# Performance work log

Measured on AMD Instinct MI355X. Metric: run time of the kernel, lower is better.

Reference implementation:

```python
import jax, jax.numpy as jnp
import numpy as np

B, CIN, HIN, WIN = 8192, 16, 6, 6
FM = 64                      # feature_maps
DK = FM // 2                 # 32
DV = FM // 2                 # 32
NH = FM // 2                 # 32 heads -> dkh = dvh = 1
OUT_CH = 5
HID = 128


def _conv2d(x, w, b, stride=1):
    # x: NCHW, w: OIHW, VALID padding (padding=(k-1)//2 = 0 for k=2)
    y = jax.lax.conv_general_dilated(
        x, w, window_strides=(stride, stride), padding='VALID',
        dimension_numbers=('NCHW', 'OIHW', 'NCHW'))
    return y + b[None, :, None, None]


def setup_inputs() -> dict:
    key = jax.random.key(0)
    ks = jax.random.split(key, 13)
    s = 0.1  # small init scale keeps softmax logits well-conditioned
    return {
        'x':      jax.random.normal(ks[0], (B, CIN, HIN, WIN), jnp.float32),
        # AugmentedConv: conv_out (out_channels - dv), qkv conv (2dk+dv), attn 1x1
        'conv_w': jax.random.normal(ks[1], (FM - DV, CIN, 2, 2), jnp.float32) * s,
        'conv_b': jax.random.normal(ks[2], (FM - DV,), jnp.float32) * s,
        'qkv_w':  jax.random.normal(ks[3], (2 * DK + DV, CIN, 2, 2), jnp.float32) * s,
        'qkv_b':  jax.random.normal(ks[4], (2 * DK + DV,), jnp.float32) * s,
        'attn_w': jax.random.normal(ks[5], (DV, DV, 1, 1), jnp.float32) * s,
        'attn_b': jax.random.normal(ks[6], (DV,), jnp.float32) * s,
        # DoubleDense: fm*5*5 -> hid -> hid//2 -> out
        'w1': jax.random.normal(ks[7], (HID, FM * 5 * 5), jnp.float32) * s,
        'b1': jax.random.normal(ks[8], (HID,), jnp.float32) * s,
        'w2': jax.random.normal(ks[9], (HID // 2, HID), jnp.float32) * s,
        'b2': jax.random.normal(ks[10], (HID // 2,), jnp.float32) * s,
        'w3': jax.random.normal(ks[11], (OUT_CH, HID // 2), jnp.float32) * s,
        'b3': jax.random.normal(ks[12], (OUT_CH,), jnp.float32) * s,
    }


def _forward(x, conv_w, conv_b, qkv_w, qkv_b, attn_w, attn_b, w1, b1, w2, b2, w3, b3):
    # ---- AugmentedConv ----
    conv_out = _conv2d(x, conv_w, conv_b)            # [B, FM-DV, 5, 5]
    qkv = _conv2d(x, qkv_w, qkv_b)                   # [B, 2DK+DV, 5, 5]
    b, _, h, w = qkv.shape
    q, k, v = jnp.split(qkv, [DK, 2 * DK], axis=1)
    dkh = DK // NH
    q = q * (dkh ** -0.5)
    flat_q = q.reshape(b, NH, dkh, h * w)            # [B, Nh, dkh, HW]
    flat_k = k.reshape(b, NH, dkh, h * w)
    flat_v = v.reshape(b, NH, DV // NH, h * w)
    # logits = q^T k over head-dim: [B, Nh, HW, HW]
    logits = jnp.einsum('bndi,bndj->bnij', flat_q, flat_k)
    weights = jax.nn.softmax(logits, axis=-1)
    # attn = weights @ v^T -> [B, Nh, HW, dvh]
    attn = jnp.einsum('bnij,bnjd->bnid', weights, flat_v.transpose(0, 1, 3, 2))
    # faithful to torch: raw reshape (B, Nh, dvh, H, W) then combine heads
    attn = attn.reshape(b, NH, DV // NH, h, w).reshape(b, DV, h, w)
    attn = _conv2d(attn, attn_w, attn_b)             # 1x1 conv
    y = jnp.concatenate([conv_out, attn], axis=1)    # [B, FM, 5, 5]
    # ---- ReLU + DoubleDense ----
    y = jax.nn.relu(y).reshape(b, -1)                # [B, FM*25]
    y = jax.nn.relu(y @ w1.T + b1)
    y = jax.nn.relu(y @ w2.T + b2)
    return y @ w3.T + b3                             # [B, OUT_CH]


def reference(x, conv_w, conv_b, qkv_w, qkv_b, attn_w, attn_b, w1, b1, w2, b2, w3, b3):
    return _forward(x, conv_w, conv_b, qkv_w, qkv_b, attn_w, attn_b,
                    w1, b1, w2, b2, w3, b3)
```

## Files before the change

kernel.cpp:

```cpp
#include <hip/hip_runtime.h>
#include <hip/hip_bf16.h>
#include <cstdint>
#include <cstddef>


typedef __attribute__((ext_vector_type(4))) float f32x4;
typedef __attribute__((ext_vector_type(2))) float f32x2;
typedef __attribute__((ext_vector_type(8))) __bf16 bf16x8;
typedef __attribute__((ext_vector_type(4))) __bf16 bf16x4;

#define LOG2E 1.4426950408889634f
#define ACT_STRIDE 1608
#define ACT_LDS_BYTES (32 * ACT_STRIDE * 2)
#define LDS_TOTAL (ACT_LDS_BYTES + 8 * 7168)

__device__ __forceinline__ float fast_exp2(float x) {
#if __has_builtin(__builtin_amdgcn_exp2f)
  return __builtin_amdgcn_exp2f(x);
#else
  return __expf(x * 0.6931471805599453f);
#endif
}

__device__ __forceinline__ f32x4 mfma16(bf16x8 a, bf16x8 b, f32x4 c) {
  return __builtin_amdgcn_mfma_f32_16x16x32_bf16(a, b, c, 0, 0, 0);
}

__global__ __launch_bounds__(64) void prep(
    const float* __restrict__ conv_w, const float* __restrict__ conv_b,
    const float* __restrict__ qkv_w,  const float* __restrict__ qkv_b,
    const float* __restrict__ attn_w,
    const float* __restrict__ w1, const float* __restrict__ w2,
    __hip_bfloat16* __restrict__ wqb, float* __restrict__ biasb,
    __hip_bfloat16* __restrict__ wab,
    __hip_bfloat16* __restrict__ w1bp, __hip_bfloat16* __restrict__ w2b) {
  const int t = threadIdx.x, tb = blockIdx.x;
  if (tb < 16) {
#pragma unroll
    for (int j = 0; j < 8; ++j) {
      int i = tb * 512 + j * 64 + t;
      float w = (i < 2048) ? conv_w[i] : qkv_w[i - 2048];
      if (i >= 4096 && i < 6144) w *= LOG2E;
      wqb[i] = __float2bfloat16(w);
    }
  } else if (tb == 16) {
#pragma unroll
    for (int j = 0; j < 16; ++j) wab[j * 64 + t] = __float2bfloat16(attn_w[j * 64 + t]);
    for (int i = t; i < 128; i += 64) {
      float b = (i < 32) ? conv_b[i] : qkv_b[i - 32];
      if (i >= 64 && i < 96) b *= LOG2E;
      biasb[i] = b;
    }
  } else if (tb < 145) {
    const int u = tb - 17;
    __shared__ float rowf[1600];
    const float* wr = w1 + u * 1600;
#pragma unroll
    for (int j = 0; j < 25; ++j) rowf[j * 64 + t] = wr[j * 64 + t];
    __hip_bfloat16* wo = w1bp + u * 1600;
#pragma unroll
    for (int j = 0; j < 25; ++j) {
      wo[j * 64 + t] = __float2bfloat16(rowf[t * 25 + j]);
    }
  } else {
#pragma unroll
    for (int j = 0; j < 64; ++j) {
      int i = (tb - 145) * 4096 + j * 64 + t;
      w2b[i] = __float2bfloat16(w2[i]);
    }
  }
}

__global__ __launch_bounds__(512) void kf(
    const float* __restrict__ x,
    const float* __restrict__ biasb,
    const __hip_bfloat16* __restrict__ wqb,
    const __hip_bfloat16* __restrict__ wab, const float* __restrict__ attn_b,
    const __hip_bfloat16* __restrict__ w1bp, const float* __restrict__ b1,
    const __hip_bfloat16* __restrict__ w2b, const float* __restrict__ b2,
    const float* __restrict__ w3, const float* __restrict__ b3,
    float* __restrict__ out) {
  extern __shared__ __align__(16) char lds_all[];
  const int t = threadIdx.x & 63;
  const int wv = threadIdx.x >> 6;
  const int l15 = t & 15, quad = t >> 4;

  __hip_bfloat16* act_lds = (__hip_bfloat16*)lds_all;
  char* my = lds_all + ACT_LDS_BYTES + wv * 7168;
  __bf16* xs  = (__bf16*)my;
  __bf16* as_ = (__bf16*)my;
  __bf16* qs  = (__bf16*)(my + 1600);

  bf16x8 bfr[8][2];
#pragma unroll
  for (int nt = 0; nt < 8; ++nt)
#pragma unroll
    for (int ks = 0; ks < 2; ++ks)
      bfr[nt][ks] = *(const bf16x8*)((const __bf16*)wqb + (nt * 16 + l15) * 64 + ks * 32 + quad * 8);
  float bias[8];
#pragma unroll
  for (int nt = 0; nt < 8; ++nt) bias[nt] = biasb[nt * 16 + l15];
  bf16x8 bw[2]; float ab[2];
#pragma unroll
  for (int nt2 = 0; nt2 < 2; ++nt2) {
    int nn = nt2 * 16 + l15;
    bw[nt2] = *(const bf16x8*)((const __bf16*)wab + nn * 32 + quad * 8);
    ab[nt2] = attn_b[nn];
  }

  const int b_base = blockIdx.x * 32 + wv * 4;
  const int n = t & 31, half = t >> 5;
  const int i0 = half * 12;

  float xr[9];
  {
    const float* xb = x + (size_t)b_base * 576;
#pragma unroll
    for (int i = 0; i < 9; ++i) xr[i] = xb[t + i * 64];
  }

#pragma unroll 1
  for (int it = 0; it < 4; ++it) {
    const int rowoff = (wv * 4 + it) * ACT_STRIDE;

#pragma unroll
    for (int i = 0; i < 9; ++i) xs[t + i * 64] = __float2bfloat16(xr[i]);

    {
      const float* xb = x + (size_t)(b_base + (it < 3 ? it + 1 : 3)) * 576;
#pragma unroll
      for (int i = 0; i < 9; ++i) xr[i] = xb[t + i * 64];
    }

#pragma unroll
    for (int mt = 0; mt < 2; ++mt) {
      int row = mt * 16 + l15;
      int pos = row < 24 ? row : 24;
      int ii = pos / 5, jj = pos - ii * 5;
      const __bf16* xp = xs + ii * 6 + jj;
      bf16x8 af[2];
#pragma unroll
      for (int ks = 0; ks < 2; ++ks) {
        const __bf16* p0 = xp + (ks * 8 + quad * 2) * 36;
        bf16x8 a;
        a[0] = p0[0];  a[1] = p0[1];  a[2] = p0[6];  a[3] = p0[7];
        a[4] = p0[36]; a[5] = p0[37]; a[6] = p0[42]; a[7] = p0[43];
        af[ks] = a;
      }
      f32x4 acc[8];
#pragma unroll
      for (int nt = 0; nt < 8; ++nt) acc[nt] = (f32x4){0.f, 0.f, 0.f, 0.f};
#pragma unroll
      for (int ks = 0; ks < 2; ++ks)
#pragma unroll
        for (int nt = 0; nt < 8; ++nt)
          acc[nt] = mfma16(af[ks], bfr[nt][ks], acc[nt]);

#pragma unroll
      for (int r = 0; r < 4; ++r) {
        int orow = mt * 16 + quad * 4 + r;
        if (orow < 25) {
#pragma unroll
          for (int nt = 0; nt < 8; ++nt) {
            float v = acc[nt][r] + bias[nt];
            if (nt < 2) {
              act_lds[rowoff + orow * 64 + nt * 16 + l15] =
                  __float2bfloat16(fmaxf(v, 0.f));
            } else {
              qs[((nt - 2) * 16 + l15) * 28 + orow] = __float2bfloat16(v);
            }
          }
        }
      }
    }

    {
      const __bf16* qp = qs + n * 28 + i0;
      const __bf16* kp = qs + (32 + n) * 28;
      const __bf16* vp = qs + (64 + n) * 28;
      f32x2 kl2[12], vv2[12];
      float kl24, vv24;
#pragma unroll
      for (int c4 = 0; c4 < 6; ++c4) {
        bf16x4 bb = *(const bf16x4*)(kp + c4 * 4);
        bf16x4 cc = *(const bf16x4*)(vp + c4 * 4);
        kl2[c4 * 2]     = (f32x2){(float)bb[0], (float)bb[1]};
        kl2[c4 * 2 + 1] = (f32x2){(float)bb[2], (float)bb[3]};
        vv2[c4 * 2]     = (f32x2){(float)cc[0], (float)cc[1]};
        vv2[c4 * 2 + 1] = (f32x2){(float)cc[2], (float)cc[3]};
      }
      kl24 = (float)kp[24]; vv24 = (float)vp[24];

      float qcur = (float)qp[0];
#pragma unroll 1
      for (int z = 0; z < 13; ++z) {
        const float qi = qcur;
        qcur = (float)qp[z + 1];
        const f32x2 qi2 = {qi, qi};
        f32x2 sA = {0.f, 0.f}, sB = {0.f, 0.f};
        f32x2 oA = {0.f, 0.f}, oB = {0.f, 0.f};
        float s4 = 0.f, o4 = 0.f;
#pragma unroll
        for (int p = 0; p < 6; ++p) {
          f32x2 mA = qi2 * kl2[p];
          f32x2 mB = qi2 * kl2[p + 6];
          f32x2 eA = {fast_exp2(mA.x), fast_exp2(mA.y)};
          f32x2 eB = {fast_exp2(mB.x), fast_exp2(mB.y)};
          sA += eA;
          sB += eB;
          oA = eA * vv2[p] + oA;
          oB = eB * vv2[p + 6] + oB;
        }
        {
          float e = fast_exp2(qi * kl24);
          s4 += e;
          o4 = __builtin_fmaf(e, vv24, o4);
        }
        float ss = ((sA.x + sA.y) + (sB.x + sB.y)) + s4;
        float oo = ((oA.x + oA.y) + (oB.x + oB.y)) + o4;
        as_[(i0 + z) * 32 + n] = __float2bfloat16(oo * __builtin_amdgcn_rcpf(ss));
      }
    }

    {
#pragma unroll
      for (int mt = 0; mt < 2; ++mt) {
        int row = mt * 16 + l15;
        int rc = row < 24 ? row : 24;
        bf16x8 af = *(const bf16x8*)(as_ + rc * 32 + quad * 8);
        f32x4 acc[2];
#pragma unroll
        for (int nt2 = 0; nt2 < 2; ++nt2)
          acc[nt2] = mfma16(af, bw[nt2], (f32x4){0.f, 0.f, 0.f, 0.f});
#pragma unroll
        for (int r = 0; r < 4; ++r) {
          int orow = mt * 16 + quad * 4 + r;
          if (orow < 25) {
#pragma unroll
            for (int nt2 = 0; nt2 < 2; ++nt2)
              act_lds[rowoff + orow * 64 + 32 + nt2 * 16 + l15] =
                  __float2bfloat16(fmaxf(acc[nt2][r] + ab[nt2], 0.f));
          }
        }
      }
    }
  }

  __syncthreads();

  const int wave = threadIdx.x >> 6;
  const int wm = wave >> 2;
  const int wn = wave & 3;
  const int b0 = blockIdx.x * 32;

  __hip_bfloat16* C1s = (__hip_bfloat16*)(lds_all + ACT_LDS_BYTES);
  __hip_bfloat16* C2s = (__hip_bfloat16*)(lds_all + ACT_LDS_BYTES + 8704);

  f32x4 acc0 = {0.f, 0.f, 0.f, 0.f};
  f32x4 acc1 = {0.f, 0.f, 0.f, 0.f};
  {
    const __bf16* aL    = (const __bf16*)act_lds + (wm * 16 + l15) * ACT_STRIDE + quad * 8;
    const __bf16* bptr0 = (const __bf16*)w1bp + (size_t)(wn * 32 + l15) * 1600 + quad * 8;
    const __bf16* bptr1 = bptr0 + 16 * 1600;
#pragma unroll 5
    for (int k0 = 0; k0 < 1600; k0 += 32) {
      bf16x8 av  = *(const bf16x8*)(aL + k0);
      bf16x8 bv0 = *(const bf16x8*)(bptr0 + k0);
      bf16x8 bv1 = *(const bf16x8*)(bptr1 + k0);
      acc0 = mfma16(av, bv0, acc0);
      acc1 = mfma16(av, bv1, acc1);
    }
  }
  {
    const int col0 = wn * 32 + l15;
    const float bias0 = b1[col0];
    const float bias1 = b1[col0 + 16];
#pragma unroll
    for (int r = 0; r < 4; ++r) {
      const int row = wm * 16 + quad * 4 + r;
      C1s[row * 136 + col0]      = __float2bfloat16(fmaxf(acc0[r] + bias0, 0.f));
      C1s[row * 136 + col0 + 16] = __float2bfloat16(fmaxf(acc1[r] + bias1, 0.f));
    }
  }
  __syncthreads();

  f32x4 acc2 = {0.f, 0.f, 0.f, 0.f};
  {
    const __bf16* aL = (const __bf16*)C1s + (wm * 16 + l15) * 136 + quad * 8;
    const __bf16* bL = (const __bf16*)w2b + (wn * 16 + l15) * 128 + quad * 8;
#pragma unroll
    for (int k0 = 0; k0 < 128; k0 += 32)
      acc2 = mfma16(*(const bf16x8*)(aL + k0), *(const bf16x8*)(bL + k0), acc2);
  }
  {
    const int col = wn * 16 + l15;
    const float bias = b2[col];
#pragma unroll
    for (int r = 0; r < 4; ++r) {
      const int row = wm * 16 + quad * 4 + r;
      C2s[row * 72 + col] = __float2bfloat16(fmaxf(acc2[r] + bias, 0.f));
    }
  }
  __syncthreads();

  if (threadIdx.x < 160) {
    const int row = threadIdx.x / 5;
    const int oc = threadIdx.x - row * 5;
    float s = b3[oc];
#pragma unroll
    for (int k = 0; k < 64; ++k)
      s += __bfloat162float(C2s[row * 72 + k]) * w3[oc * 64 + k];
    out[(size_t)(b0 + row) * 5 + oc] = s;
  }
}

extern "C" void kernel_launch(void* const* d_in, const int* in_sizes, int n_in,
                              void* d_out, int out_size, void* d_ws, size_t ws_size,
                              hipStream_t stream) {
  const float* x      = (const float*)d_in[0];
  const float* conv_w = (const float*)d_in[1];
  const float* conv_b = (const float*)d_in[2];
  const float* qkv_w  = (const float*)d_in[3];
  const float* qkv_b  = (const float*)d_in[4];
  const float* attn_w = (const float*)d_in[5];
  const float* attn_b = (const float*)d_in[6];
  const float* w1 = (const float*)d_in[7];
  const float* b1 = (const float*)d_in[8];
  const float* w2 = (const float*)d_in[9];
  const float* b2 = (const float*)d_in[10];
  const float* w3 = (const float*)d_in[11];
  const float* b3 = (const float*)d_in[12];
  float* out = (float*)d_out;

  char* ws = (char*)d_ws;
  __hip_bfloat16* w1bp  = (__hip_bfloat16*)ws;
  __hip_bfloat16* w2b   = (__hip_bfloat16*)(ws + 409600);
  __hip_bfloat16* wqb   = (__hip_bfloat16*)(ws + 425984);
  float*          biasb = (float*)(ws + 442368);
  __hip_bfloat16* wab   = (__hip_bfloat16*)(ws + 442880);

  hipFuncSetAttribute(reinterpret_cast<const void*>(kf),
                      hipFuncAttributeMaxDynamicSharedMemorySize, LDS_TOTAL);

  prep<<<dim3(147), dim3(64), 0, stream>>>(conv_w, conv_b, qkv_w, qkv_b, attn_w,
                                           w1, w2, wqb, biasb, wab, w1bp, w2b);
  kf<<<dim3(256), dim3(512), LDS_TOTAL, stream>>>(x, biasb, wqb, wab, attn_b,
                                                  w1bp, b1, w2b, b2, w3, b3, out);
}
```

Baseline: 152.3 us.

## Halve per-block batch tile, shuffle K/V via bpermute, reload weights per iteration

```diff
diff --git a/kernel.cpp b/kernel.cpp
--- a/kernel.cpp
+++ b/kernel.cpp
@@ -11,8 +11,9 @@
 
 #define LOG2E 1.4426950408889634f
 #define ACT_STRIDE 1608
-#define ACT_LDS_BYTES (32 * ACT_STRIDE * 2)
-#define LDS_TOTAL (ACT_LDS_BYTES + 8 * 7168)
+#define ACT_LDS_BYTES (16 * ACT_STRIDE * 2)
+#define SCRATCH_PER_WAVE 3456
+#define LDS_TOTAL (ACT_LDS_BYTES + 8 * SCRATCH_PER_WAVE)
 
 __device__ __forceinline__ float fast_exp2(float x) {
 #if __has_builtin(__builtin_amdgcn_exp2f)
@@ -24,6 +25,16 @@
 
 __device__ __forceinline__ f32x4 mfma16(bf16x8 a, bf16x8 b, f32x4 c) {
   return __builtin_amdgcn_mfma_f32_16x16x32_bf16(a, b, c, 0, 0, 0);
+}
+
+__device__ __forceinline__ unsigned pack2(float lo, float hi) {
+  unsigned short a = __builtin_bit_cast(unsigned short, __float2bfloat16(lo));
+  unsigned short b = __builtin_bit_cast(unsigned short, __float2bfloat16(hi));
+  return ((unsigned)b << 16) | (unsigned)a;
+}
+
+__device__ __forceinline__ float bsel(int u, unsigned lsh) {
+  return __builtin_bit_cast(float, (((unsigned)u) << lsh) & 0xffff0000u);
 }
 
 __global__ __launch_bounds__(64) void prep(
@@ -71,7 +82,7 @@
   }
 }
 
-__global__ __launch_bounds__(512) void kf(
+__global__ __launch_bounds__(512, 4) void kf(
     const float* __restrict__ x,
     const float* __restrict__ biasb,
     const __hip_bfloat16* __restrict__ wqb,
@@ -86,17 +97,11 @@
   const int l15 = t & 15, quad = t >> 4;
 
   __hip_bfloat16* act_lds = (__hip_bfloat16*)lds_all;
-  char* my = lds_all + ACT_LDS_BYTES + wv * 7168;
-  __bf16* xs  = (__bf16*)my;
-  __bf16* as_ = (__bf16*)my;
-  __bf16* qs  = (__bf16*)(my + 1600);
-
-  bf16x8 bfr[8][2];
-#pragma unroll
-  for (int nt = 0; nt < 8; ++nt)
-#pragma unroll
-    for (int ks = 0; ks < 2; ++ks)
-      bfr[nt][ks] = *(const bf16x8*)((const __bf16*)wqb + (nt * 16 + l15) * 64 + ks * 32 + quad * 8);
+  char* my = lds_all + ACT_LDS_BYTES + wv * SCRATCH_PER_WAVE;
+  __bf16* qs  = (__bf16*)my;
+  __bf16* xs  = (__bf16*)(my + 1792);
+  __bf16* as_ = (__bf16*)(my + 1792);
+
   float bias[8];
 #pragma unroll
   for (int nt = 0; nt < 8; ++nt) bias[nt] = biasb[nt * 16 + l15];
@@ -108,9 +113,11 @@
     ab[nt2] = attn_b[nn];
   }
 
-  const int b_base = blockIdx.x * 32 + wv * 4;
+  const int b_base = blockIdx.x * 16 + wv * 2;
   const int n = t & 31, half = t >> 5;
   const int i0 = half * 12;
+  const int bp0 = (n & 15) * 4;
+  const unsigned lsh = (n & 16) ? 0u : 16u;
 
   float xr[9];
   {
@@ -120,18 +127,26 @@
   }
 
 #pragma unroll 1
-  for (int it = 0; it < 4; ++it) {
-    const int rowoff = (wv * 4 + it) * ACT_STRIDE;
+  for (int it = 0; it < 2; ++it) {
+    const int rowoff = (wv * 2 + it) * ACT_STRIDE;
 
 #pragma unroll
     for (int i = 0; i < 9; ++i) xs[t + i * 64] = __float2bfloat16(xr[i]);
 
-    {
-      const float* xb = x + (size_t)(b_base + (it < 3 ? it + 1 : 3)) * 576;
+    bf16x8 bfr[8][2];
+#pragma unroll
+    for (int nt = 0; nt < 8; ++nt)
+#pragma unroll
+      for (int ks = 0; ks < 2; ++ks)
+        bfr[nt][ks] = *(const bf16x8*)((const __bf16*)wqb + (nt * 16 + l15) * 64 + ks * 32 + quad * 8);
+
+    if (it == 0) {
+      const float* xb = x + (size_t)(b_base + 1) * 576;
 #pragma unroll
       for (int i = 0; i < 9; ++i) xr[i] = xb[t + i * 64];
     }
 
+    unsigned pkK[2][4], pkV[2][4];
 #pragma unroll
     for (int mt = 0; mt < 2; ++mt) {
       int row = mt * 16 + l15;
@@ -161,7 +176,7 @@
         int orow = mt * 16 + quad * 4 + r;
         if (orow < 25) {
 #pragma unroll
-          for (int nt = 0; nt < 8; ++nt) {
+          for (int nt = 0; nt < 4; ++nt) {
             float v = acc[nt][r] + bias[nt];
             if (nt < 2) {
               act_lds[rowoff + orow * 64 + nt * 16 + l15] =
@@ -171,26 +186,27 @@
             }
           }
         }
+        pkK[mt][r] = pack2(acc[4][r] + bias[4], acc[5][r] + bias[5]);
+        pkV[mt][r] = pack2(acc[6][r] + bias[6], acc[7][r] + bias[7]);
       }
     }
+
+    f32x2 kl2[12], vv2[12];
+#pragma unroll
+    for (int c = 0; c < 12; ++c) {
+      const int j0 = 2 * c, j1 = 2 * c + 1;
+      int uk0 = __builtin_amdgcn_ds_bpermute(bp0 + 64 * ((j0 >> 2) & 3), (int)pkK[j0 >> 4][j0 & 3]);
+      int uk1 = __builtin_amdgcn_ds_bpermute(bp0 + 64 * ((j1 >> 2) & 3), (int)pkK[j1 >> 4][j1 & 3]);
+      int uv0 = __builtin_amdgcn_ds_bpermute(bp0 + 64 * ((j0 >> 2) & 3), (int)pkV[j0 >> 4][j0 & 3]);
+      int uv1 = __builtin_amdgcn_ds_bpermute(bp0 + 64 * ((j1 >> 2) & 3), (int)pkV[j1 >> 4][j1 & 3]);
+      kl2[c] = (f32x2){bsel(uk0, lsh), bsel(uk1, lsh)};
+      vv2[c] = (f32x2){bsel(uv0, lsh), bsel(uv1, lsh)};
+    }
+    const float kl24 = bsel(__builtin_amdgcn_ds_bpermute(bp0 + 128, (int)pkK[1][0]), lsh);
+    const float vv24 = bsel(__builtin_amdgcn_ds_bpermute(bp0 + 128, (int)pkV[1][0]), lsh);
 
     {
       const __bf16* qp = qs + n * 28 + i0;
-      const __bf16* kp = qs + (32 + n) * 28;
-      const __bf16* vp = qs + (64 + n) * 28;
-      f32x2 kl2[12], vv2[12];
-      float kl24, vv24;
-#pragma unroll
-      for (int c4 = 0; c4 < 6; ++c4) {
-        bf16x4 bb = *(const bf16x4*)(kp + c4 * 4);
-        bf16x4 cc = *(const bf16x4*)(vp + c4 * 4);
-        kl2[c4 * 2]     = (f32x2){(float)bb[0], (float)bb[1]};
-        kl2[c4 * 2 + 1] = (f32x2){(float)bb[2], (float)bb[3]};
-        vv2[c4 * 2]     = (f32x2){(float)cc[0], (float)cc[1]};
-        vv2[c4 * 2 + 1] = (f32x2){(float)cc[2], (float)cc[3]};
-      }
-      kl24 = (float)kp[24]; vv24 = (float)vp[24];
-
       float qcur = (float)qp[0];
 #pragma unroll 1
       for (int z = 0; z < 13; ++z) {
@@ -249,61 +265,47 @@
   __syncthreads();
 
   const int wave = threadIdx.x >> 6;
-  const int wm = wave >> 2;
-  const int wn = wave & 3;
-  const int b0 = blockIdx.x * 32;
+  const int b0 = blockIdx.x * 16;
 
   __hip_bfloat16* C1s = (__hip_bfloat16*)(lds_all + ACT_LDS_BYTES);
-  __hip_bfloat16* C2s = (__hip_bfloat16*)(lds_all + ACT_LDS_BYTES + 8704);
-
-  f32x4 acc0 = {0.f, 0.f, 0.f, 0.f};
-  f32x4 acc1 = {0.f, 0.f, 0.f, 0.f};
+  __hip_bfloat16* C2s = (__hip_bfloat16*)(lds_all + ACT_LDS_BYTES + 4352);
+
   {
-    const __bf16* aL    = (const __bf16*)act_lds + (wm * 16 + l15) * ACT_STRIDE + quad * 8;
-    const __bf16* bptr0 = (const __bf16*)w1bp + (size_t)(wn * 32 + l15) * 1600 + quad * 8;
-    const __bf16* bptr1 = bptr0 + 16 * 1600;
+    f32x4 acc0 = {0.f, 0.f, 0.f, 0.f};
+    f32x4 acc1 = {0.f, 0.f, 0.f, 0.f};
+    const __bf16* aL   = (const __bf16*)act_lds + l15 * ACT_STRIDE + quad * 8;
+    const __bf16* bptr = (const __bf16*)w1bp + (size_t)(wave * 16 + l15) * 1600 + quad * 8;
 #pragma unroll 5
-    for (int k0 = 0; k0 < 1600; k0 += 32) {
-      bf16x8 av  = *(const bf16x8*)(aL + k0);
-      bf16x8 bv0 = *(const bf16x8*)(bptr0 + k0);
-      bf16x8 bv1 = *(const bf16x8*)(bptr1 + k0);
-      acc0 = mfma16(av, bv0, acc0);
-      acc1 = mfma16(av, bv1, acc1);
-    }
-  }
-  {
-    const int col0 = wn * 32 + l15;
-    const float bias0 = b1[col0];
-    const float bias1 = b1[col0 + 16];
+    for (int k0 = 0; k0 < 1600; k0 += 64) {
+      acc0 = mfma16(*(const bf16x8*)(aL + k0),      *(const bf16x8*)(bptr + k0),      acc0);
+      acc1 = mfma16(*(const bf16x8*)(aL + k0 + 32), *(const bf16x8*)(bptr + k0 + 32), acc1);
+    }
+    const int col = wave * 16 + l15;
+    const float bias1 = b1[col];
 #pragma unroll
     for (int r = 0; r < 4; ++r) {
-      const int row = wm * 16 + quad * 4 + r;
-      C1s[row * 136 + col0]      = __float2bfloat16(fmaxf(acc0[r] + bias0, 0.f));
-      C1s[row * 136 + col0 + 16] = __float2bfloat16(fmaxf(acc1[r] + bias1, 0.f));
+      C1s[(quad * 4 + r) * 136 + col] =
+          __float2bfloat16(fmaxf(acc0[r] + acc1[r] + bias1, 0.f));
     }
   }
   __syncthreads();
 
-  f32x4 acc2 = {0.f, 0.f, 0.f, 0.f};
-  {
-    const __bf16* aL = (const __bf16*)C1s + (wm * 16 + l15) * 136 + quad * 8;
-    const __bf16* bL = (const __bf16*)w2b + (wn * 16 + l15) * 128 + quad * 8;
+  if (wave < 4) {
+    f32x4 acc2 = {0.f, 0.f, 0.f, 0.f};
+    const __bf16* aL = (const __bf16*)C1s + l15 * 136 + quad * 8;
+    const __bf16* bL = (const __bf16*)w2b + (wave * 16 + l15) * 128 + quad * 8;
 #pragma unroll
     for (int k0 = 0; k0 < 128; k0 += 32)
       acc2 = mfma16(*(const bf16x8*)(aL + k0), *(const bf16x8*)(bL + k0), acc2);
-  }
-  {
-    const int col = wn * 16 + l15;
+    const int col = wave * 16 + l15;
     const float bias = b2[col];
 #pragma unroll
-    for (int r = 0; r < 4; ++r) {
-      const int row = wm * 16 + quad * 4 + r;
-      C2s[row * 72 + col] = __float2bfloat16(fmaxf(acc2[r] + bias, 0.f));
-    }
+    for (int r = 0; r < 4; ++r)
+      C2s[(quad * 4 + r) * 72 + col] = __float2bfloat16(fmaxf(acc2[r] + bias, 0.f));
   }
   __syncthreads();
 
-  if (threadIdx.x < 160) {
+  if (threadIdx.x < 80) {
     const int row = threadIdx.x / 5;
     const int oc = threadIdx.x - row * 5;
     float s = b3[oc];
@@ -344,6 +346,6 @@
 
   prep<<<dim3(147), dim3(64), 0, stream>>>(conv_w, conv_b, qkv_w, qkv_b, attn_w,
                                            w1, w2, wqb, biasb, wab, w1bp, w2b);
-  kf<<<dim3(256), dim3(512), LDS_TOTAL, stream>>>(x, biasb, wqb, wab, attn_b,
+  kf<<<dim3(512), dim3(512), LDS_TOTAL, stream>>>(x, biasb, wqb, wab, attn_b,
                                                   w1bp, b1, w2b, b2, w3, b3, out);
 }
```

New measurement: 195.3 us. +28.3%, slower.
